# Optimization experiments

Measured on AMD Instinct MI355X. Metric: run time of the kernel, lower is better.

## Reference

```python
import jax, jax.numpy as jnp
import numpy as np

B, S, D, H, F = 4, 1024, 1024, 16, 4096
DH = D // H  # 64


def _xavier(key, shape):
    fan_in, fan_out = shape[-2], shape[-1]
    limit = np.sqrt(6.0 / (fan_in + fan_out)).astype(np.float32)
    return jax.random.uniform(key, shape, jnp.float32, -limit, limit)


def setup_inputs() -> dict:
    key = jax.random.key(0)
    ks = jax.random.split(key, 24)
    inp = {
        'decoder_input': jax.random.normal(ks[0], (B, S, D), jnp.float32),
        'encoder_output': jax.random.normal(ks[1], (B, S, D), jnp.float32),
        'mask': jnp.broadcast_to(jnp.tril(jnp.ones((S, S), jnp.bool_)), (B, S, S)),
    }
    # self-attention per-head Q/K/V weights stacked over heads: (H, D, DH)
    for i, p in enumerate(['sa', 'ca']):
        base = 2 + i * 8
        inp[f'{p}_wq'] = _xavier(ks[base + 0], (H, D, DH))
        inp[f'{p}_wk'] = _xavier(ks[base + 1], (H, D, DH))
        inp[f'{p}_wv'] = _xavier(ks[base + 2], (H, D, DH))
        inp[f'{p}_bq'] = jnp.zeros((H, DH), jnp.float32)
        inp[f'{p}_bk'] = jnp.zeros((H, DH), jnp.float32)
        inp[f'{p}_bv'] = jnp.zeros((H, DH), jnp.float32)
        inp[f'{p}_wo'] = _xavier(ks[base + 3], (H * DH, D))
        inp[f'{p}_bo'] = jnp.zeros((D,), jnp.float32)
    inp['ff_w1'] = _xavier(ks[18], (D, F))
    inp['ff_b1'] = jnp.zeros((F,), jnp.float32)
    inp['ff_w2'] = _xavier(ks[19], (F, D))
    inp['ff_b2'] = jnp.zeros((D,), jnp.float32)
    for j in (1, 2, 3):
        inp[f'ln{j}_g'] = jnp.ones((D,), jnp.float32)
        inp[f'ln{j}_b'] = jnp.zeros((D,), jnp.float32)
    return inp


def _layernorm(x, g, b, eps=1e-12):
    # torch x.var() default is unbiased (ddof=1) -- match it
    mean = jnp.mean(x, axis=-1, keepdims=True)
    var = jnp.var(x, axis=-1, keepdims=True, ddof=1)
    return g * (x - mean) * jax.lax.rsqrt(var + eps) + b


def _mha(q_in, k_in, v_in, wq, bq, wk, bk, wv, bv, wo, bo, mask=None):
    scale = np.float32(1.0 / np.sqrt(DH))
    q = jnp.einsum('bsd,hde->bhse', q_in, wq) + bq[None, :, None, :]
    k = jnp.einsum('bsd,hde->bhse', k_in, wk) + bk[None, :, None, :]
    v = jnp.einsum('bsd,hde->bhse', v_in, wv) + bv[None, :, None, :]
    scores = jnp.einsum('bhqe,bhke->bhqk', q, k) * scale
    if mask is not None:
        scores = jnp.where(mask[:, None, :, :], scores, jnp.float32(-1e9))
    attn = jax.nn.softmax(scores, axis=-1)
    out = jnp.einsum('bhqk,bhke->bhqe', attn, v)  # (B,H,S,DH)
    out = out.transpose(0, 2, 1, 3).reshape(q_in.shape[0], q_in.shape[1], H * DH)
    return out @ wo + bo


def reference(decoder_input, encoder_output, mask,
              sa_wq, sa_wk, sa_wv, sa_bq, sa_bk, sa_bv, sa_wo, sa_bo,
              ca_wq, ca_wk, ca_wv, ca_bq, ca_bk, ca_bv, ca_wo, ca_bo,
              ff_w1, ff_b1, ff_w2, ff_b2,
              ln1_g, ln1_b, ln2_g, ln2_b, ln3_g, ln3_b):
    # dropout is identity (eval mode)
    out1 = _mha(decoder_input, decoder_input, decoder_input,
                sa_wq, sa_bq, sa_wk, sa_bk, sa_wv, sa_bv, sa_wo, sa_bo, mask)
    out1 = _layernorm(out1 + decoder_input, ln1_g, ln1_b)
    out2 = _mha(out1, encoder_output, encoder_output,
                ca_wq, ca_bq, ca_wk, ca_bk, ca_wv, ca_bv, ca_wo, ca_bo, None)
    out2 = _layernorm(out2 + out1, ln2_g, ln2_b)
    out3 = jax.nn.relu(out2 @ ff_w1 + ff_b1) @ ff_w2 + ff_b2
    out3 = _layernorm(out3 + out2, ln3_g, ln3_b)
    return out3
```

## Files before the change

### kernel.cpp

```cpp
#include <hip/hip_runtime.h>
#include <hip/hip_bf16.h>

using bf16 = __hip_bfloat16;
typedef __attribute__((ext_vector_type(8))) short bf16x8;
typedef __attribute__((ext_vector_type(4))) float f32x4;

__device__ __forceinline__ float toF(float x) { return x; }
__device__ __forceinline__ float toF(bf16 x) { return __bfloat162float(x); }

template <typename T> __device__ __forceinline__ T fromF(float x);
template <> __device__ __forceinline__ float fromF<float>(float x) { return x; }
template <> __device__ __forceinline__ bf16 fromF<bf16>(float x) { return __float2bfloat16(x); }

__device__ __forceinline__ unsigned short f2bu(float f) {
    bf16 h = __float2bfloat16(f);
    return *reinterpret_cast<unsigned short*>(&h);
}

__device__ __forceinline__ void gload16(const unsigned short* g, unsigned short* l) {
    __builtin_amdgcn_global_load_lds(
        (const __attribute__((address_space(1))) unsigned int*)g,
        (__attribute__((address_space(3))) unsigned int*)l, 16, 0, 0);
}

__global__ __launch_bounds__(256) void cvt_k(const float* __restrict__ X,
                                             unsigned short* __restrict__ Y, int n)
{
    int i = (blockIdx.x * 256 + threadIdx.x) * 4;
    if (i >= n) return;
    float4 v = *(const float4*)(X + i);
    ushort4 o;
    o.x = f2bu(v.x); o.y = f2bu(v.y); o.z = f2bu(v.z); o.w = f2bu(v.w);
    *(ushort4*)(Y + i) = o;
}

template <bool HEADED>
__global__ __launch_bounds__(256) void wtrans_k(
    const float* __restrict__ W, unsigned short* __restrict__ Wt, int K, int N)
{
    __shared__ float t[32][33];
    const int k0 = blockIdx.x * 32, n0 = blockIdx.y * 32;
    const int tx = threadIdx.x & 31, ty = threadIdx.x >> 5;
#pragma unroll
    for (int i = 0; i < 4; i++) {
        int k = k0 + ty + 8 * i, n = n0 + tx;
        float v;
        if constexpr (HEADED) v = W[((size_t)(n >> 6) * K + k) * 64 + (n & 63)];
        else                  v = W[(size_t)k * N + n];
        t[ty + 8 * i][tx] = v;
    }
    __syncthreads();
#pragma unroll
    for (int i = 0; i < 4; i++)
        Wt[(size_t)(n0 + ty + 8 * i) * K + k0 + tx] = f2bu(t[tx][ty + 8 * i]);
}

template <typename TO, typename TR, bool RELU, bool HASRES, int BN>
__global__ __launch_bounds__(256) void gemm_mfma(
    const unsigned short* __restrict__ A, const unsigned short* __restrict__ Bt,
    const float* __restrict__ bias, const TR* __restrict__ res,
    TO* __restrict__ C, int M, int N, int K)
{
    constexpr int MI = (BN == 128) ? 4 : 2;
    __shared__ __align__(16) unsigned short As[128 * 64];
    __shared__ __align__(16) unsigned short Bs[BN * 64];

    const int tid = threadIdx.x;
    const int lane = tid & 63, wv = tid >> 6;
    const int quad = lane >> 4, col = lane & 15;
    const int m0 = blockIdx.y * 128, n0 = blockIdx.x * BN;
    const int wm = (BN == 128) ? (wv >> 1) * 64 : wv * 32;
    const int wn = (BN == 128) ? (wv & 1) * 64 : 0;

    f32x4 acc[MI][4];
#pragma unroll
    for (int i = 0; i < MI; i++)
#pragma unroll
        for (int j = 0; j < 4; j++) acc[i][j] = (f32x4){0.f, 0.f, 0.f, 0.f};

    const int rowl = (wv << 3) + (lane >> 3);
    const int xq = (lane & 7) ^ (lane >> 3);
    const unsigned short* Ag = A + (size_t)(m0 + rowl) * K + xq * 8;
    const unsigned short* Bg = Bt + (size_t)(n0 + rowl) * K + xq * 8;
    unsigned short* AsW = As + wv * 512;
    unsigned short* BsW = Bs + wv * 512;

    const int xr = col & 7;

    for (int k0 = 0; k0 < K; k0 += 64) {
        __syncthreads();
#pragma unroll
        for (int r = 0; r < 4; r++)
            gload16(Ag + (size_t)(r * 32) * K + k0, AsW + r * 2048);
#pragma unroll
        for (int r = 0; r < BN / 32; r++)
            gload16(Bg + (size_t)(r * 32) * K + k0, BsW + r * 2048);
        __syncthreads();

#pragma unroll
        for (int kk = 0; kk < 2; kk++) {
            const int cq = ((kk << 2) + quad) ^ xr;
            bf16x8 af[MI], bfr[4];
#pragma unroll
            for (int mi = 0; mi < MI; mi++)
                af[mi] = *(const bf16x8*)(As + (wm + mi * 16 + col) * 64 + cq * 8);
#pragma unroll
            for (int ni = 0; ni < 4; ni++)
                bfr[ni] = *(const bf16x8*)(Bs + (wn + ni * 16 + col) * 64 + cq * 8);
#pragma unroll
            for (int mi = 0; mi < MI; mi++)
#pragma unroll
                for (int ni = 0; ni < 4; ni++)
                    acc[mi][ni] = __builtin_amdgcn_mfma_f32_16x16x32_bf16(
                        af[mi], bfr[ni], acc[mi][ni], 0, 0, 0);
        }
    }

    float bv[4];
#pragma unroll
    for (int ni = 0; ni < 4; ni++) bv[ni] = bias[n0 + wn + ni * 16 + col];
#pragma unroll
    for (int mi = 0; mi < MI; mi++) {
#pragma unroll
        for (int r = 0; r < 4; r++) {
            int m = m0 + wm + mi * 16 + quad * 4 + r;
#pragma unroll
            for (int ni = 0; ni < 4; ni++) {
                int n = n0 + wn + ni * 16 + col;
                float v = acc[mi][ni][r] + bv[ni];
                if constexpr (HASRES) v += toF(res[(size_t)m * N + n]);
                if constexpr (RELU) v = v > 0.f ? v : 0.f;
                C[(size_t)m * N + n] = fromF<TO>(v);
            }
        }
    }
}

struct SegArgs {
    const float* bias[3];
    unsigned short* out[3];
};

__global__ __launch_bounds__(256) void gemm_seg(
    const unsigned short* __restrict__ A, const unsigned short* __restrict__ Bt,
    SegArgs sp, int M, int K, int transSeg)
{
    __shared__ __align__(16) unsigned short As[128 * 64];
    __shared__ __align__(16) unsigned short Bs[128 * 64];

    const int tid = threadIdx.x;
    const int lane = tid & 63, wv = tid >> 6;
    const int quad = lane >> 4, col = lane & 15;
    const int m0 = blockIdx.y * 128, n0 = blockIdx.x * 128;
    const int wm = (wv >> 1) * 64, wn = (wv & 1) * 64;

    f32x4 acc[4][4];
#pragma unroll
    for (int i = 0; i < 4; i++)
#pragma unroll
        for (int j = 0; j < 4; j++) acc[i][j] = (f32x4){0.f, 0.f, 0.f, 0.f};

    const int rowl = (wv << 3) + (lane >> 3);
    const int xq = (lane & 7) ^ (lane >> 3);
    const unsigned short* Ag = A + (size_t)(m0 + rowl) * K + xq * 8;
    const unsigned short* Bg = Bt + (size_t)(n0 + rowl) * K + xq * 8;
    unsigned short* AsW = As + wv * 512;
    unsigned short* BsW = Bs + wv * 512;
    const int xr = col & 7;

    for (int k0 = 0; k0 < K; k0 += 64) {
        __syncthreads();
#pragma unroll
        for (int r = 0; r < 4; r++)
            gload16(Ag + (size_t)(r * 32) * K + k0, AsW + r * 2048);
#pragma unroll
        for (int r = 0; r < 4; r++)
            gload16(Bg + (size_t)(r * 32) * K + k0, BsW + r * 2048);
        __syncthreads();

#pragma unroll
        for (int kk = 0; kk < 2; kk++) {
            const int cq = ((kk << 2) + quad) ^ xr;
            bf16x8 af[4], bfr[4];
#pragma unroll
            for (int mi = 0; mi < 4; mi++)
                af[mi] = *(const bf16x8*)(As + (wm + mi * 16 + col) * 64 + cq * 8);
#pragma unroll
            for (int ni = 0; ni < 4; ni++)
                bfr[ni] = *(const bf16x8*)(Bs + (wn + ni * 16 + col) * 64 + cq * 8);
#pragma unroll
            for (int mi = 0; mi < 4; mi++)
#pragma unroll
                for (int ni = 0; ni < 4; ni++)
                    acc[mi][ni] = __builtin_amdgcn_mfma_f32_16x16x32_bf16(
                        af[mi], bfr[ni], acc[mi][ni], 0, 0, 0);
        }
    }

    const int seg = n0 >> 10;
    const float* bias = sp.bias[seg];
    unsigned short* out = sp.out[seg];
    const int nb = (n0 & 1023) + wn;
    const bool trans = (seg == transSeg);

    float bv[4];
#pragma unroll
    for (int ni = 0; ni < 4; ni++) bv[ni] = bias[nb + ni * 16 + col];
#pragma unroll
    for (int mi = 0; mi < 4; mi++) {
#pragma unroll
        for (int r = 0; r < 4; r++) {
            int m = m0 + wm + mi * 16 + quad * 4 + r;
#pragma unroll
            for (int ni = 0; ni < 4; ni++) {
                int nl = nb + ni * 16 + col;
                float v = acc[mi][ni][r] + bv[ni];
                if (trans)
                    out[((size_t)(m >> 10) * 1024 + nl) * 1024 + (m & 1023)] = f2bu(v);
                else
                    out[(size_t)m * 1024 + nl] = f2bu(v);
            }
        }
    }
}

template <bool CAUSAL>
__global__ __launch_bounds__(256) void fattn_k(
    const unsigned short* __restrict__ Q, const unsigned short* __restrict__ K,
    const unsigned short* __restrict__ Vt, unsigned short* __restrict__ O, int S)
{
    const int qt = blockIdx.x, h = blockIdx.y, b = blockIdx.z;
    const int H64 = 1024;
    const int tid = threadIdx.x;
    const int w = tid >> 6, lane = tid & 63;
    const int quad = lane >> 4, col = lane & 15;

    __shared__ __align__(16) unsigned short Ks[64 * 72];
    __shared__ __align__(16) unsigned short Vs[64 * 72];
    __shared__ __align__(16) unsigned short Ps[4 * 16 * 72];

    const int qBase = qt * 64 + w * 16;
    const size_t qrow = ((size_t)b * S + qBase + col) * H64 + h * 64;
    const bf16x8 qf0 = *(const bf16x8*)(Q + qrow + quad * 8);
    const bf16x8 qf1 = *(const bf16x8*)(Q + qrow + quad * 8 + 32);

    f32x4 o[4];
#pragma unroll
    for (int g = 0; g < 4; g++) o[g] = (f32x4){0.f, 0.f, 0.f, 0.f};
    float m_run[4], l_run[4];
#pragma unroll
    for (int r = 0; r < 4; r++) { m_run[r] = -1e30f; l_run[r] = 0.f; }

    const int skey = tid >> 2;
    const int sseg = (tid & 3) * 16;
    const size_t kgbase = (size_t)b * S * H64 + h * 64;
    const size_t vgbase = ((size_t)b * 1024 + h * 64) * (size_t)S;

    const int nkt = CAUSAL ? (qt + 1) : (S >> 6);
    const float scale = 0.125f;
    unsigned short* Pw = Ps + w * (16 * 72);

    for (int kt = 0; kt < nkt; kt++) {
        __syncthreads();
        {
            const unsigned short* kg_ = K + kgbase + (size_t)(kt * 64 + skey) * H64;
            const unsigned short* vg_ = Vt + vgbase + (size_t)skey * S + kt * 64;
            *(uint4*)(Ks + skey * 72 + sseg)     = *(const uint4*)(kg_ + sseg);
            *(uint4*)(Ks + skey * 72 + sseg + 8) = *(const uint4*)(kg_ + sseg + 8);
            *(uint4*)(Vs + skey * 72 + sseg)     = *(const uint4*)(vg_ + sseg);
            *(uint4*)(Vs + skey * 72 + sseg + 8) = *(const uint4*)(vg_ + sseg + 8);
        }
        __syncthreads();

        f32x4 s[4];
#pragma unroll
        for (int kg = 0; kg < 4; kg++) {
            bf16x8 k0 = *(const bf16x8*)(Ks + (kg * 16 + col) * 72 + quad * 8);
            bf16x8 k1 = *(const bf16x8*)(Ks + (kg * 16 + col) * 72 + quad * 8 + 32);
            f32x4 a = (f32x4){0.f, 0.f, 0.f, 0.f};
            a = __builtin_amdgcn_mfma_f32_16x16x32_bf16(qf0, k0, a, 0, 0, 0);
            a = __builtin_amdgcn_mfma_f32_16x16x32_bf16(qf1, k1, a, 0, 0, 0);
            s[kg] = a;
        }

#pragma unroll
        for (int kg = 0; kg < 4; kg++)
#pragma unroll
            for (int r = 0; r < 4; r++) {
                float v = s[kg][r] * scale;
                if (CAUSAL) {
                    int key = kt * 64 + kg * 16 + col;
                    int q = qBase + quad * 4 + r;
                    if (key > q) v = -1e30f;
                }
                s[kg][r] = v;
            }

#pragma unroll
        for (int r = 0; r < 4; r++) {
            float mx = fmaxf(fmaxf(s[0][r], s[1][r]), fmaxf(s[2][r], s[3][r]));
#pragma unroll
            for (int off = 1; off < 16; off <<= 1)
                mx = fmaxf(mx, __shfl_xor(mx, off));
            float mnew = fmaxf(m_run[r], mx);
            float ps = 0.f;
#pragma unroll
            for (int kg = 0; kg < 4; kg++) {
                float e = __expf(s[kg][r] - mnew);
                s[kg][r] = e;
                ps += e;
            }
#pragma unroll
            for (int off = 1; off < 16; off <<= 1)
                ps += __shfl_xor(ps, off);
            float alpha = __expf(m_run[r] - mnew);
            l_run[r] = l_run[r] * alpha + ps;
            m_run[r] = mnew;
#pragma unroll
            for (int g = 0; g < 4; g++) o[g][r] *= alpha;
        }

#pragma unroll
        for (int kg = 0; kg < 4; kg++)
#pragma unroll
            for (int r = 0; r < 4; r++)
                Pw[(quad * 4 + r) * 72 + kg * 16 + col] = f2bu(s[kg][r]);
        __syncthreads();

        bf16x8 p0 = *(const bf16x8*)(Pw + col * 72 + quad * 8);
        bf16x8 p1 = *(const bf16x8*)(Pw + col * 72 + quad * 8 + 32);

#pragma unroll
        for (int g = 0; g < 4; g++) {
            bf16x8 v0 = *(const bf16x8*)(Vs + (g * 16 + col) * 72 + quad * 8);
            bf16x8 v1 = *(const bf16x8*)(Vs + (g * 16 + col) * 72 + quad * 8 + 32);
            o[g] = __builtin_amdgcn_mfma_f32_16x16x32_bf16(p0, v0, o[g], 0, 0, 0);
            o[g] = __builtin_amdgcn_mfma_f32_16x16x32_bf16(p1, v1, o[g], 0, 0, 0);
        }
    }

    const size_t orow = ((size_t)b * S + qBase) * H64 + h * 64;
#pragma unroll
    for (int r = 0; r < 4; r++) {
        float inv = 1.f / l_run[r];
        int q = quad * 4 + r;
#pragma unroll
        for (int g = 0; g < 4; g++)
            O[orow + (size_t)q * H64 + g * 16 + col] = f2bu(o[g][r] * inv);
    }
}

template <typename TO>
__global__ __launch_bounds__(256) void ln_k(
    const float* __restrict__ X, const float* __restrict__ g,
    const float* __restrict__ bb, TO* __restrict__ O, int D)
{
    const int row = blockIdx.x;
    const int tid = threadIdx.x;
    __shared__ float xs[1024];
    __shared__ float red[256];
    const float* x = X + (size_t)row * D;

    float s = 0.f;
    for (int i = tid; i < D; i += 256) { float v = x[i]; xs[i] = v; s += v; }
    red[tid] = s;
    __syncthreads();
    for (int t = 128; t > 0; t >>= 1) {
        if (tid < t) red[tid] += red[tid + t];
        __syncthreads();
    }
    const float mean = red[0] / (float)D;
    __syncthreads();

    float s2 = 0.f;
    for (int i = tid; i < D; i += 256) { float d = xs[i] - mean; s2 += d * d; }
    red[tid] = s2;
    __syncthreads();
    for (int t = 128; t > 0; t >>= 1) {
        if (tid < t) red[tid] += red[tid + t];
        __syncthreads();
    }
    const float rstd = rsqrtf(red[0] / (float)(D - 1) + 1e-12f);

    TO* o = O + (size_t)row * D;
    for (int i = tid; i < D; i += 256)
        o[i] = fromF<TO>(g[i] * (xs[i] - mean) * rstd + bb[i]);
}

extern "C" void kernel_launch(void* const* d_in, const int* in_sizes, int n_in,
                              void* d_out, int out_size, void* d_ws, size_t ws_size,
                              hipStream_t stream)
{
    const int Bb = 4, S = 1024, D = 1024, F = 4096;
    const int M = Bb * S;
    const int H = 16;

    const float* dec = (const float*)d_in[0];
    const float* enc = (const float*)d_in[1];

    int base = 2;
    if (n_in >= 29 && in_sizes[2] == Bb * S * S) base = 3;

    const float* sa_wq = (const float*)d_in[base + 0];
    const float* sa_wk = (const float*)d_in[base + 1];
    const float* sa_wv = (const float*)d_in[base + 2];
    const float* sa_bq = (const float*)d_in[base + 3];
    const float* sa_bk = (const float*)d_in[base + 4];
    const float* sa_bv = (const float*)d_in[base + 5];
    const float* sa_wo = (const float*)d_in[base + 6];
    const float* sa_bo = (const float*)d_in[base + 7];
    const float* ca_wq = (const float*)d_in[base + 8];
    const float* ca_wk = (const float*)d_in[base + 9];
    const float* ca_wv = (const float*)d_in[base + 10];
    const float* ca_bq = (const float*)d_in[base + 11];
    const float* ca_bk = (const float*)d_in[base + 12];
    const float* ca_bv = (const float*)d_in[base + 13];
    const float* ca_wo = (const float*)d_in[base + 14];
    const float* ca_bo = (const float*)d_in[base + 15];
    const float* ff_w1 = (const float*)d_in[base + 16];
    const float* ff_b1 = (const float*)d_in[base + 17];
    const float* ff_w2 = (const float*)d_in[base + 18];
    const float* ff_b2 = (const float*)d_in[base + 19];
    const float* ln1_g = (const float*)d_in[base + 20];
    const float* ln1_b = (const float*)d_in[base + 21];
    const float* ln2_g = (const float*)d_in[base + 22];
    const float* ln2_b = (const float*)d_in[base + 23];
    const float* ln3_g = (const float*)d_in[base + 24];
    const float* ln3_b = (const float*)d_in[base + 25];

    const size_t E = (size_t)M * D;
    const size_t M1 = (size_t)1024 * 1024;
    float* SUM = (float*)d_ws;
    bf16* O1 = (bf16*)(SUM + E);
    bf16* O2 = O1 + E;
    bf16* Q  = O2 + E;
    bf16* Kb = Q + E;
    bf16* Vt = Kb + E;
    bf16* AO = Vt + E;
    bf16* HID = Q;
    unsigned short* decB = (unsigned short*)AO;
    unsigned short* Wt   = (unsigned short*)d_out;
    unsigned short* encB = (unsigned short*)d_out + 4 * 1024 * 1024;

    dim3 blk(256);
    dim3 gQKV(3 * D / 128, M / 128);
    dim3 gKV(2 * D / 128, M / 128);
    dim3 gN(D / 64, M / 128);
    dim3 gF(F / 128, M / 128);
    dim3 gA(S / 64, H, Bb);
    dim3 gT(D / 32, D / 32);
    dim3 gT1(D / 32, F / 32);
    dim3 gT2(F / 32, D / 32);

    cvt_k<<<M * D / 1024, blk, 0, stream>>>(dec, decB, M * D);
    cvt_k<<<M * D / 1024, blk, 0, stream>>>(enc, encB, M * D);

    wtrans_k<true><<<gT, blk, 0, stream>>>(sa_wq, Wt, D, D);
    wtrans_k<true><<<gT, blk, 0, stream>>>(sa_wk, Wt + M1, D, D);
    wtrans_k<true><<<gT, blk, 0, stream>>>(sa_wv, Wt + 2 * M1, D, D);
    {
        SegArgs sp;
        sp.bias[0] = sa_bq; sp.bias[1] = sa_bk; sp.bias[2] = sa_bv;
        sp.out[0] = (unsigned short*)Q; sp.out[1] = (unsigned short*)Kb;
        sp.out[2] = (unsigned short*)Vt;
        gemm_seg<<<gQKV, blk, 0, stream>>>(decB, Wt, sp, M, D, 2);
    }
    fattn_k<true><<<gA, blk, 0, stream>>>((const unsigned short*)Q, (const unsigned short*)Kb,
                                          (const unsigned short*)Vt, (unsigned short*)AO, S);
    wtrans_k<false><<<gT, blk, 0, stream>>>(sa_wo, Wt, D, D);
    gemm_mfma<float, float, false, true, 64><<<gN, blk, 0, stream>>>(
        (const unsigned short*)AO, Wt, sa_bo, dec, SUM, M, D, D);
    ln_k<bf16><<<M, blk, 0, stream>>>(SUM, ln1_g, ln1_b, O1, D);

    wtrans_k<true><<<gT, blk, 0, stream>>>(ca_wq, Wt, D, D);
    gemm_mfma<bf16, float, false, false, 64><<<gN, blk, 0, stream>>>(
        (const unsigned short*)O1, Wt, ca_bq, (const float*)nullptr, Q, M, D, D);
    wtrans_k<true><<<gT, blk, 0, stream>>>(ca_wk, Wt, D, D);
    wtrans_k<true><<<gT, blk, 0, stream>>>(ca_wv, Wt + M1, D, D);
    {
        SegArgs sp;
        sp.bias[0] = ca_bk; sp.bias[1] = ca_bv; sp.bias[2] = nullptr;
        sp.out[0] = (unsigned short*)Kb; sp.out[1] = (unsigned short*)Vt;
        sp.out[2] = nullptr;
        gemm_seg<<<gKV, blk, 0, stream>>>(encB, Wt, sp, M, D, 1);
    }
    fattn_k<false><<<gA, blk, 0, stream>>>((const unsigned short*)Q, (const unsigned short*)Kb,
                                           (const unsigned short*)Vt, (unsigned short*)AO, S);
    wtrans_k<false><<<gT, blk, 0, stream>>>(ca_wo, Wt, D, D);
    gemm_mfma<float, bf16, false, true, 64><<<gN, blk, 0, stream>>>(
        (const unsigned short*)AO, Wt, ca_bo, O1, SUM, M, D, D);
    ln_k<bf16><<<M, blk, 0, stream>>>(SUM, ln2_g, ln2_b, O2, D);

    wtrans_k<false><<<gT1, blk, 0, stream>>>(ff_w1, Wt, D, F);
    gemm_mfma<bf16, float, true, false, 128><<<gF, blk, 0, stream>>>(
        (const unsigned short*)O2, Wt, ff_b1, (const float*)nullptr, HID, M, F, D);
    wtrans_k<false><<<gT2, blk, 0, stream>>>(ff_w2, Wt, F, D);
    gemm_mfma<float, bf16, false, true, 64><<<gN, blk, 0, stream>>>(
        (const unsigned short*)HID, Wt, ff_b2, O2, SUM, M, D, F);
    ln_k<float><<<M, blk, 0, stream>>>(SUM, ln3_g, ln3_b, (float*)d_out, D);
}
```

Measured before the change: 610.9 us.

## Streamline flash attention softmax and batch weight transposes into fewer launches

The attention kernel now folds the 1/sqrt(d) scale and log2(e) into Q once, so it can use exp2f and skip the per-element multiply. It applies the causal mask only on the diagonal tile and skips the running-max rescale when the new max stays within a threshold (a lazy rescale). Causal blocks are issued in reverse order so the longest tiles start first, balancing the load. The per-weight transpose launches are merged into one launch per group by indexing blockIdx.z, which cuts launch overhead. Rounding Q to bf16 after scaling and the deferred rescale add small numerical risk, including possible overflow if scores jump more than the threshold.

```diff
diff --git a/kernel.cpp b/kernel.cpp
--- a/kernel.cpp
+++ b/kernel.cpp
@@ -15,6 +15,10 @@
 __device__ __forceinline__ unsigned short f2bu(float f) {
     bf16 h = __float2bfloat16(f);
     return *reinterpret_cast<unsigned short*>(&h);
+}
+__device__ __forceinline__ float bu2f(unsigned short u) {
+    unsigned int x = ((unsigned int)u) << 16;
+    return __uint_as_float(x);
 }
 
 __device__ __forceinline__ void gload16(const unsigned short* g, unsigned short* l) {
@@ -34,11 +38,15 @@
     *(ushort4*)(Y + i) = o;
 }
 
+struct WPtrs { const float* w[3]; };
+
 template <bool HEADED>
 __global__ __launch_bounds__(256) void wtrans_k(
-    const float* __restrict__ W, unsigned short* __restrict__ Wt, int K, int N)
+    WPtrs wp, unsigned short* __restrict__ Wt, int K, int N)
 {
     __shared__ float t[32][33];
+    const float* __restrict__ W = wp.w[blockIdx.z];
+    unsigned short* __restrict__ out = Wt + (size_t)blockIdx.z * K * N;
     const int k0 = blockIdx.x * 32, n0 = blockIdx.y * 32;
     const int tx = threadIdx.x & 31, ty = threadIdx.x >> 5;
 #pragma unroll
@@ -52,7 +60,7 @@
     __syncthreads();
 #pragma unroll
     for (int i = 0; i < 4; i++)
-        Wt[(size_t)(n0 + ty + 8 * i) * K + k0 + tx] = f2bu(t[tx][ty + 8 * i]);
+        out[(size_t)(n0 + ty + 8 * i) * K + k0 + tx] = f2bu(t[tx][ty + 8 * i]);
 }
 
 template <typename TO, typename TR, bool RELU, bool HASRES, int BN>
@@ -229,7 +237,8 @@
     const unsigned short* __restrict__ Q, const unsigned short* __restrict__ K,
     const unsigned short* __restrict__ Vt, unsigned short* __restrict__ O, int S)
 {
-    const int qt = blockIdx.x, h = blockIdx.y, b = blockIdx.z;
+    const int qt = CAUSAL ? ((int)gridDim.x - 1 - (int)blockIdx.x) : blockIdx.x;
+    const int h = blockIdx.y, b = blockIdx.z;
     const int H64 = 1024;
     const int tid = threadIdx.x;
     const int w = tid >> 6, lane = tid & 63;
@@ -241,8 +250,18 @@
 
     const int qBase = qt * 64 + w * 16;
     const size_t qrow = ((size_t)b * S + qBase + col) * H64 + h * 64;
-    const bf16x8 qf0 = *(const bf16x8*)(Q + qrow + quad * 8);
-    const bf16x8 qf1 = *(const bf16x8*)(Q + qrow + quad * 8 + 32);
+
+    const float qscale = 0.125f * 1.44269504f;
+    bf16x8 qf0, qf1;
+    {
+        bf16x8 r0 = *(const bf16x8*)(Q + qrow + quad * 8);
+        bf16x8 r1 = *(const bf16x8*)(Q + qrow + quad * 8 + 32);
+#pragma unroll
+        for (int j = 0; j < 8; j++) {
+            qf0[j] = (short)f2bu(bu2f((unsigned short)r0[j]) * qscale);
+            qf1[j] = (short)f2bu(bu2f((unsigned short)r1[j]) * qscale);
+        }
+    }
 
     f32x4 o[4];
 #pragma unroll
@@ -257,7 +276,6 @@
     const size_t vgbase = ((size_t)b * 1024 + h * 64) * (size_t)S;
 
     const int nkt = CAUSAL ? (qt + 1) : (S >> 6);
-    const float scale = 0.125f;
     unsigned short* Pw = Ps + w * (16 * 72);
 
     for (int kt = 0; kt < nkt; kt++) {
@@ -283,41 +301,54 @@
             s[kg] = a;
         }
 
-#pragma unroll
-        for (int kg = 0; kg < 4; kg++)
+        if (CAUSAL && kt == qt) {
+#pragma unroll
+            for (int kg = 0; kg < 4; kg++)
+#pragma unroll
+                for (int r = 0; r < 4; r++) {
+                    int key = kg * 16 + col;
+                    int q = w * 16 + quad * 4 + r;
+                    if (key > q) s[kg][r] = -1e30f;
+                }
+        }
+
+        float mx[4];
+#pragma unroll
+        for (int r = 0; r < 4; r++) {
+            float m2 = fmaxf(fmaxf(s[0][r], s[1][r]), fmaxf(s[2][r], s[3][r]));
+#pragma unroll
+            for (int off = 1; off < 16; off <<= 1)
+                m2 = fmaxf(m2, __shfl_xor(m2, off));
+            mx[r] = m2;
+        }
+
+        bool defer = (mx[0] <= m_run[0] + 8.f) & (mx[1] <= m_run[1] + 8.f)
+                   & (mx[2] <= m_run[2] + 8.f) & (mx[3] <= m_run[3] + 8.f);
+        if (!__all(defer)) {
 #pragma unroll
             for (int r = 0; r < 4; r++) {
-                float v = s[kg][r] * scale;
-                if (CAUSAL) {
-                    int key = kt * 64 + kg * 16 + col;
-                    int q = qBase + quad * 4 + r;
-                    if (key > q) v = -1e30f;
-                }
-                s[kg][r] = v;
+                float mnew = fmaxf(m_run[r], mx[r]);
+                float alpha = exp2f(m_run[r] - mnew);
+                l_run[r] *= alpha;
+#pragma unroll
+                for (int g = 0; g < 4; g++) o[g][r] *= alpha;
+                m_run[r] = mnew;
             }
+        }
 
 #pragma unroll
         for (int r = 0; r < 4; r++) {
-            float mx = fmaxf(fmaxf(s[0][r], s[1][r]), fmaxf(s[2][r], s[3][r]));
-#pragma unroll
-            for (int off = 1; off < 16; off <<= 1)
-                mx = fmaxf(mx, __shfl_xor(mx, off));
-            float mnew = fmaxf(m_run[r], mx);
             float ps = 0.f;
 #pragma unroll
             for (int kg = 0; kg < 4; kg++) {
-                float e = __expf(s[kg][r] - mnew);
+                float e = exp2f(s[kg][r] - m_run[r]);
                 s[kg][r] = e;
                 ps += e;
             }
 #pragma unroll
             for (int off = 1; off < 16; off <<= 1)
                 ps += __shfl_xor(ps, off);
-            float alpha = __expf(m_run[r] - mnew);
-            l_run[r] = l_run[r] * alpha + ps;
-            m_run[r] = mnew;
-#pragma unroll
-            for (int g = 0; g < 4; g++) o[g][r] *= alpha;
+            l_run[r] += ps;
         }
 
 #pragma unroll
@@ -448,16 +479,19 @@
     dim3 gN(D / 64, M / 128);
     dim3 gF(F / 128, M / 128);
     dim3 gA(S / 64, H, Bb);
-    dim3 gT(D / 32, D / 32);
-    dim3 gT1(D / 32, F / 32);
-    dim3 gT2(F / 32, D / 32);
+    dim3 gT3(D / 32, D / 32, 3);
+    dim3 gT2z(D / 32, D / 32, 2);
+    dim3 gT(D / 32, D / 32, 1);
+    dim3 gT1(D / 32, F / 32, 1);
+    dim3 gT2(F / 32, D / 32, 1);
 
     cvt_k<<<M * D / 1024, blk, 0, stream>>>(dec, decB, M * D);
     cvt_k<<<M * D / 1024, blk, 0, stream>>>(enc, encB, M * D);
 
-    wtrans_k<true><<<gT, blk, 0, stream>>>(sa_wq, Wt, D, D);
-    wtrans_k<true><<<gT, blk, 0, stream>>>(sa_wk, Wt + M1, D, D);
-    wtrans_k<true><<<gT, blk, 0, stream>>>(sa_wv, Wt + 2 * M1, D, D);
+    {
+        WPtrs wp; wp.w[0] = sa_wq; wp.w[1] = sa_wk; wp.w[2] = sa_wv;
+        wtrans_k<true><<<gT3, blk, 0, stream>>>(wp, Wt, D, D);
+    }
     {
         SegArgs sp;
         sp.bias[0] = sa_bq; sp.bias[1] = sa_bk; sp.bias[2] = sa_bv;
@@ -467,16 +501,24 @@
     }
     fattn_k<true><<<gA, blk, 0, stream>>>((const unsigned short*)Q, (const unsigned short*)Kb,
                                           (const unsigned short*)Vt, (unsigned short*)AO, S);
-    wtrans_k<false><<<gT, blk, 0, stream>>>(sa_wo, Wt, D, D);
+    {
+        WPtrs wp; wp.w[0] = sa_wo; wp.w[1] = nullptr; wp.w[2] = nullptr;
+        wtrans_k<false><<<gT, blk, 0, stream>>>(wp, Wt, D, D);
+    }
     gemm_mfma<float, float, false, true, 64><<<gN, blk, 0, stream>>>(
         (const unsigned short*)AO, Wt, sa_bo, dec, SUM, M, D, D);
     ln_k<bf16><<<M, blk, 0, stream>>>(SUM, ln1_g, ln1_b, O1, D);
 
-    wtrans_k<true><<<gT, blk, 0, stream>>>(ca_wq, Wt, D, D);
+    {
+        WPtrs wp; wp.w[0] = ca_wq; wp.w[1] = nullptr; wp.w[2] = nullptr;
+        wtrans_k<true><<<gT, blk, 0, stream>>>(wp, Wt, D, D);
+    }
     gemm_mfma<bf16, float, false, false, 64><<<gN, blk, 0, stream>>>(
         (const unsigned short*)O1, Wt, ca_bq, (const float*)nullptr, Q, M, D, D);
-    wtrans_k<true><<<gT, blk, 0, stream>>>(ca_wk, Wt, D, D);
-    wtrans_k<true><<<gT, blk, 0, stream>>>(ca_wv, Wt + M1, D, D);
+    {
+        WPtrs wp; wp.w[0] = ca_wk; wp.w[1] = ca_wv; wp.w[2] = nullptr;
+        wtrans_k<true><<<gT2z, blk, 0, stream>>>(wp, Wt, D, D);
+    }
     {
         SegArgs sp;
         sp.bias[0] = ca_bk; sp.bias[1] = ca_bv; sp.bias[2] = nullptr;
@@ -486,15 +528,24 @@
     }
     fattn_k<false><<<gA, blk, 0, stream>>>((const unsigned short*)Q, (const unsigned short*)Kb,
                                            (const unsigned short*)Vt, (unsigned short*)AO, S);
-    wtrans_k<false><<<gT, blk, 0, stream>>>(ca_wo, Wt, D, D);
+    {
+        WPtrs wp; wp.w[0] = ca_wo; wp.w[1] = nullptr; wp.w[2] = nullptr;
+        wtrans_k<false><<<gT, blk, 0, stream>>>(wp, Wt, D, D);
+    }
     gemm_mfma<float, bf16, false, true, 64><<<gN, blk, 0, stream>>>(
         (const unsigned short*)AO, Wt, ca_bo, O1, SUM, M, D, D);
     ln_k<bf16><<<M, blk, 0, stream>>>(SUM, ln2_g, ln2_b, O2, D);
 
-    wtrans_k<false><<<gT1, blk, 0, stream>>>(ff_w1, Wt, D, F);
+    {
+        WPtrs wp; wp.w[0] = ff_w1; wp.w[1] = nullptr; wp.w[2] = nullptr;
+        wtrans_k<false><<<gT1, blk, 0, stream>>>(wp, Wt, D, F);
+    }
     gemm_mfma<bf16, float, true, false, 128><<<gF, blk, 0, stream>>>(
         (const unsigned short*)O2, Wt, ff_b1, (const float*)nullptr, HID, M, F, D);
-    wtrans_k<false><<<gT2, blk, 0, stream>>>(ff_w2, Wt, F, D);
+    {
+        WPtrs wp; wp.w[0] = ff_w2; wp.w[1] = nullptr; wp.w[2] = nullptr;
+        wtrans_k<false><<<gT2, blk, 0, stream>>>(wp, Wt, F, D);
+    }
     gemm_mfma<float, bf16, false, true, 64><<<gN, blk, 0, stream>>>(
         (const unsigned short*)HID, Wt, ff_b2, O2, SUM, M, D, F);
     ln_k<float><<<M, blk, 0, stream>>>(SUM, ln3_g, ln3_b, (float*)d_out, D);
```

New measurement: 600.8 us. About the same (-1.6%).
